# Optimization experiments

Measured on AMD Instinct MI355X. Metric: run time of the kernel, lower is better.

The kernel has to match this reference:

```python
import jax, jax.numpy as jnp
import numpy as np

D_IN = 768
D_OUT = 768
NUM_HEADS = 12
HEAD_DIM = D_OUT // NUM_HEADS


def setup_inputs() -> dict:
    key = jax.random.key(0)
    ks = jax.random.split(key, 6)
    s = 1.0 / np.sqrt(D_IN)
    X = jax.random.normal(ks[0], (4, 2048, D_IN), dtype=jnp.float32)
    Wq = jax.random.uniform(ks[1], (D_IN, D_OUT), jnp.float32, -s, s)
    Wk = jax.random.uniform(ks[2], (D_IN, D_OUT), jnp.float32, -s, s)
    Wv = jax.random.uniform(ks[3], (D_IN, D_OUT), jnp.float32, -s, s)
    Wo = jax.random.uniform(ks[4], (D_OUT, D_OUT), jnp.float32, -s, s)
    bo = jax.random.uniform(ks[5], (D_OUT,), jnp.float32, -s, s)
    return {"X": X, "Wq": Wq, "Wk": Wk, "Wv": Wv, "Wo": Wo, "bo": bo}


def reference(X, Wq, Wk, Wv, Wo, bo):
    b, n, _ = X.shape
    # QKV projections, split heads -> [b, h, n, d]
    def split(t):
        return t.reshape(b, n, NUM_HEADS, HEAD_DIM).transpose(0, 2, 1, 3)
    q = split(X @ Wq)
    k = split(X @ Wk)
    v = split(X @ Wv)
    scores = jnp.einsum('bhqd,bhkd->bhqk', q, k) / np.sqrt(HEAD_DIM).astype(np.float32)
    causal = jnp.triu(jnp.ones((n, n), dtype=bool), k=1)
    scores = jnp.where(causal, -jnp.inf, scores)
    attn = jax.nn.softmax(scores, axis=-1)  # dropout p=0 -> identity
    ctx = jnp.einsum('bhqk,bhkd->bhqd', attn, v)
    ctx = ctx.transpose(0, 2, 1, 3).reshape(b, n, D_OUT)
    return ctx @ Wo + bo
```

## Files before the change

### kernel.cpp

```cpp
#include <hip/hip_runtime.h>
#include <stdint.h>

#define B_  4
#define N_  2048
#define D_  768
#define H_  12
#define HD_ 64
#define M_  (B_*N_)

typedef short bf8 __attribute__((ext_vector_type(8)));
typedef float f32x4 __attribute__((ext_vector_type(4)));

static __device__ __forceinline__ unsigned short f2bf(float f) {
    unsigned u = __float_as_uint(f);
    unsigned r = u + 0x7fffu + ((u >> 16) & 1u);
    return (unsigned short)(r >> 16);
}

static __device__ __forceinline__ unsigned pk2bf(float f0, float f1) {
    return ((__float_as_uint(f1) + 0x8000u) & 0xFFFF0000u) |
           ((__float_as_uint(f0) + 0x8000u) >> 16);
}

#if __has_builtin(__builtin_amdgcn_exp2f)
#define EXP2(x) __builtin_amdgcn_exp2f(x)
#else
#define EXP2(x) exp2f(x)
#endif

#define GLOAD_LDS16(gptr, lptr)                                                   \
    __builtin_amdgcn_global_load_lds(                                             \
        (const __attribute__((address_space(1))) void*)(gptr),                    \
        (__attribute__((address_space(3))) void*)(lptr), 16, 0, 0)

#define QSCALE 0.1803368801111204f

__global__ __launch_bounds__(256) void convert_x(const float* __restrict__ X,
                                                 unsigned short* __restrict__ Xb) {
    const size_t i = ((size_t)blockIdx.x * 256 + threadIdx.x) * 8;
    const float4 a = *(const float4*)(X + i);
    const float4 b = *(const float4*)(X + i + 4);
    ushort4 lo, hi;
    lo.x = f2bf(a.x); lo.y = f2bf(a.y); lo.z = f2bf(a.z); lo.w = f2bf(a.w);
    hi.x = f2bf(b.x); hi.y = f2bf(b.y); hi.z = f2bf(b.z); hi.w = f2bf(b.w);
    *(ushort4*)(Xb + i)     = lo;
    *(ushort4*)(Xb + i + 4) = hi;
}

__global__ __launch_bounds__(256) void transpose_w(
    const float* __restrict__ Wq, const float* __restrict__ Wk,
    const float* __restrict__ Wv, const float* __restrict__ Wo,
    unsigned short* __restrict__ Wqt, unsigned short* __restrict__ Wkt,
    unsigned short* __restrict__ Wvt, unsigned short* __restrict__ Wot)
{
    __shared__ float tile[32][33];
    const int z = blockIdx.z;
    const float* W = (z == 0) ? Wq : (z == 1) ? Wk : (z == 2) ? Wv : Wo;
    unsigned short* Wt = (z == 0) ? Wqt : (z == 1) ? Wkt : (z == 2) ? Wvt : Wot;
    const int k0 = blockIdx.x * 32, n0 = blockIdx.y * 32;
    const int tx = threadIdx.x & 31, ty = threadIdx.x >> 5;
    #pragma unroll
    for (int i = 0; i < 4; ++i)
        tile[ty + 8 * i][tx] = W[(size_t)(k0 + ty + 8 * i) * D_ + n0 + tx];
    __syncthreads();
    #pragma unroll
    for (int i = 0; i < 4; ++i)
        Wt[(size_t)(n0 + ty + 8 * i) * D_ + k0 + tx] = f2bf(tile[tx][ty + 8 * i]);
}

__global__ __launch_bounds__(256) void qkv_mfma(
    const unsigned short* __restrict__ Xb,
    const unsigned short* __restrict__ Wqt, const unsigned short* __restrict__ Wkt,
    const unsigned short* __restrict__ Wvt,
    unsigned short* __restrict__ Qb, unsigned short* __restrict__ Kb,
    unsigned short* __restrict__ Vt)
{
    __shared__ unsigned short As[8192];
    __shared__ unsigned short Bs[8192];

    const int t = threadIdx.x;
    const int wave = t >> 6, lane = t & 63;
    const int col = lane & 15, quad = lane >> 4;
    const int wm = (wave & 1) * 64, wn = (wave >> 1) * 64;

    const int orig = blockIdx.x;
    const int wgid = (orig & 7) * 144 + (orig >> 3);
    const int m0  = (wgid / 18) * 128;
    const int nm  = wgid % 18;
    const int mat = nm / 6;
    const int n0  = (nm % 6) * 128;
    const unsigned short* Wt = (mat == 0) ? Wqt : (mat == 1) ? Wkt : Wvt;
    const bool sw = (mat != 2);

    const unsigned short* Ag = Xb + (size_t)(m0 + (t >> 2)) * D_ + (t & 3) * 8;
    const unsigned short* Bg = Wt + (size_t)(n0 + (t >> 2)) * D_ + (t & 3) * 8;
    unsigned short* AsD = As + t * 8;
    unsigned short* BsD = Bs + t * 8;

    f32x4 acc[4][4] = {};

    for (int k0 = 0; k0 < D_; k0 += 64) {
        __syncthreads();
        GLOAD_LDS16(Ag + k0,                        AsD);
        GLOAD_LDS16(Ag + k0 + 32,                   AsD + 4096);
        GLOAD_LDS16(Ag + (size_t)64 * D_ + k0,      AsD + 2048);
        GLOAD_LDS16(Ag + (size_t)64 * D_ + k0 + 32, AsD + 6144);
        GLOAD_LDS16(Bg + k0,                        BsD);
        GLOAD_LDS16(Bg + k0 + 32,                   BsD + 4096);
        GLOAD_LDS16(Bg + (size_t)64 * D_ + k0,      BsD + 2048);
        GLOAD_LDS16(Bg + (size_t)64 * D_ + k0 + 32, BsD + 6144);
        __syncthreads();

        #pragma unroll
        for (int ks = 0; ks < 2; ++ks) {
            bf8 a[4], b[4];
            #pragma unroll
            for (int i = 0; i < 4; ++i)
                a[i] = *(const bf8*)(As + ks * 4096 + (wm + i * 16 + col) * 32 + quad * 8);
            #pragma unroll
            for (int j = 0; j < 4; ++j)
                b[j] = *(const bf8*)(Bs + ks * 4096 + (wn + j * 16 + col) * 32 + quad * 8);
            if (sw) {
                #pragma unroll
                for (int i = 0; i < 4; ++i)
                    #pragma unroll
                    for (int j = 0; j < 4; ++j)
                        acc[i][j] = __builtin_amdgcn_mfma_f32_16x16x32_bf16(b[j], a[i], acc[i][j], 0, 0, 0);
            } else {
                #pragma unroll
                for (int i = 0; i < 4; ++i)
                    #pragma unroll
                    for (int j = 0; j < 4; ++j)
                        acc[i][j] = __builtin_amdgcn_mfma_f32_16x16x32_bf16(a[i], b[j], acc[i][j], 0, 0, 0);
            }
        }
    }

    if (sw) {
        unsigned short* Out = (mat == 0) ? Qb : Kb;
        const float qsc = (mat == 0) ? QSCALE : 1.0f;
        #pragma unroll
        for (int i = 0; i < 4; ++i) {
            const int token = m0 + wm + i * 16 + col;
            const int bb = token >> 11, nn = token & (N_ - 1);
            #pragma unroll
            for (int j = 0; j < 4; ++j) {
                const int n = n0 + wn + j * 16 + quad * 4;
                const int h = n >> 6, d = n & 63;
                ushort4 pk;
                pk.x = f2bf(acc[i][j][0] * qsc);
                pk.y = f2bf(acc[i][j][1] * qsc);
                pk.z = f2bf(acc[i][j][2] * qsc);
                pk.w = f2bf(acc[i][j][3] * qsc);
                *(ushort4*)(Out + ((size_t)(bb * H_ + h) * N_ + nn) * HD_ + d) = pk;
            }
        }
    } else {
        #pragma unroll
        for (int j = 0; j < 4; ++j) {
            const int n = n0 + wn + j * 16 + col;
            const int h = n >> 6, d = n & 63;
            #pragma unroll
            for (int i = 0; i < 4; ++i) {
                const int mb = m0 + wm + i * 16 + quad * 4;
                const int bb = mb >> 11;
                const int nn = mb & (N_ - 1);
                const int nnp = (nn & ~31) | ((quad >> 1) << 4) | ((quad & 1) << 3) |
                                ((i & 1) << 2);
                ushort4 pk;
                pk.x = f2bf(acc[i][j][0]); pk.y = f2bf(acc[i][j][1]);
                pk.z = f2bf(acc[i][j][2]); pk.w = f2bf(acc[i][j][3]);
                *(ushort4*)(Vt + ((size_t)(bb * H_ + h) * HD_ + d) * N_ + nnp) = pk;
            }
        }
    }
}

#define PS 72

static __device__ __forceinline__ void qk_mfma8(
    const bf8 (&ka)[4][2], bf8 qb0, bf8 qb1, f32x4 (&s)[4])
{
    __builtin_amdgcn_s_setprio(1);
    #pragma unroll
    for (int kc = 0; kc < 4; ++kc) {
        s[kc] = __builtin_amdgcn_mfma_f32_16x16x32_bf16(ka[kc][0], qb0, s[kc], 0, 0, 0);
        s[kc] = __builtin_amdgcn_mfma_f32_16x16x32_bf16(ka[kc][1], qb1, s[kc], 0, 0, 0);
    }
    __builtin_amdgcn_s_setprio(0);
}

static __device__ __forceinline__ void softmax_pack(
    const f32x4 (&s)[4], int k0, int q, bool mask, float& lpart,
    bf8& pb0, bf8& pb1, int quad)
{
    float p[4][4];
    if (mask) {
        #pragma unroll
        for (int kc = 0; kc < 4; ++kc)
            #pragma unroll
            for (int r = 0; r < 4; ++r) {
                const int key = k0 + kc * 16 + quad * 4 + r;
                p[kc][r] = EXP2((key > q) ? -INFINITY : s[kc][r]);
            }
    } else {
        #pragma unroll
        for (int kc = 0; kc < 4; ++kc)
            #pragma unroll
            for (int r = 0; r < 4; ++r) p[kc][r] = EXP2(s[kc][r]);
    }

    #pragma unroll
    for (int kc = 0; kc < 4; ++kc)
        #pragma unroll
        for (int r = 0; r < 4; ++r) lpart += p[kc][r];

    uint4 u0, u1;
    u0.x = pk2bf(p[0][0], p[0][1]); u0.y = pk2bf(p[0][2], p[0][3]);
    u0.z = pk2bf(p[1][0], p[1][1]); u0.w = pk2bf(p[1][2], p[1][3]);
    u1.x = pk2bf(p[2][0], p[2][1]); u1.y = pk2bf(p[2][2], p[2][3]);
    u1.z = pk2bf(p[3][0], p[3][1]); u1.w = pk2bf(p[3][2], p[3][3]);
    pb0 = *(bf8*)&u0;
    pb1 = *(bf8*)&u1;
}

static __device__ __forceinline__ void pv_acc(
    bf8 pb0, bf8 pb1, const bf8 (&va)[4][2], f32x4 (&o)[4])
{
    __builtin_amdgcn_s_setprio(1);
    #pragma unroll
    for (int dc = 0; dc < 4; ++dc) {
        o[dc] = __builtin_amdgcn_mfma_f32_16x16x32_bf16(va[dc][0], pb0, o[dc], 0, 0, 0);
        o[dc] = __builtin_amdgcn_mfma_f32_16x16x32_bf16(va[dc][1], pb1, o[dc], 0, 0, 0);
    }
    __builtin_amdgcn_s_setprio(0);
}

__global__ __launch_bounds__(256, 3) void attn_mfma(
    const unsigned short* __restrict__ Qb,
    const unsigned short* __restrict__ Kb,
    const unsigned short* __restrict__ Vt,
    unsigned short* __restrict__ Ctxb)
{
    __shared__ unsigned short Kl[2][64 * PS];
    __shared__ unsigned short Vl[2][64 * PS];

    const int t = threadIdx.x;
    const int wave = t >> 6;
    const int lane = t & 63;
    const int col  = lane & 15;
    const int quad = lane >> 4;

    const int orig = blockIdx.x;
    const int bid  = (orig & 7) * 96 + (orig >> 3);
    const int bh  = bid >> 4;
    const int x   = bid & 15;
    const int tl  = x, th = 31 - x;
    const int q0L = tl * 64 + wave * 16;
    const int q0H = th * 64 + wave * 16;
    const int qL  = q0L + col;
    const int qH  = q0H + col;

    const unsigned short* Kp = Kb + (size_t)bh * N_ * HD_;
    const unsigned short* Vp = Vt + (size_t)bh * HD_ * N_;
    const unsigned short* QpL = Qb + ((size_t)bh * N_ + q0L) * HD_;
    const unsigned short* QpH = Qb + ((size_t)bh * N_ + q0H) * HD_;

    const bf8 qbL0 = *(const bf8*)(QpL + (size_t)col * HD_ + quad * 8);
    const bf8 qbL1 = *(const bf8*)(QpL + (size_t)col * HD_ + 32 + quad * 8);
    const bf8 qbH0 = *(const bf8*)(QpH + (size_t)col * HD_ + quad * 8);
    const bf8 qbH1 = *(const bf8*)(QpH + (size_t)col * HD_ + 32 + quad * 8);

    f32x4 oL[4] = {}, oH[4] = {};
    float lL = 0.f, lH = 0.f;

    const int srow = t >> 3;
    const int scol = (t & 7) * 8;
    const unsigned short* Kg = Kp + (size_t)srow * HD_ + scol;
    const unsigned short* Vg = Vp + (size_t)srow * N_ + scol;
    const int kO0 = srow * PS + scol;
    const int kO1 = (srow + 32) * PS + scol;

    const int iters = 32 - x;

    uint4 kr0 = *(const uint4*)(Kg);
    uint4 kr1 = *(const uint4*)(Kg + (size_t)32 * HD_);
    uint4 vr0 = *(const uint4*)(Vg);
    uint4 vr1 = *(const uint4*)(Vg + (size_t)32 * N_);
    *(uint4*)(Kl[0] + kO0) = kr0;
    *(uint4*)(Kl[0] + kO1) = kr1;
    *(uint4*)(Vl[0] + kO0) = vr0;
    *(uint4*)(Vl[0] + kO1) = vr1;
    kr0 = *(const uint4*)(Kg + (size_t)64 * HD_);
    kr1 = *(const uint4*)(Kg + (size_t)96 * HD_);
    vr0 = *(const uint4*)(Vg + 64);
    vr1 = *(const uint4*)(Vg + (size_t)32 * N_ + 64);

    for (int kt = 0; kt < iters; ++kt) {
        const int k0 = kt * 64;
        const bool actL = (kt <= tl);
        const unsigned short* Kc = Kl[kt & 1];
        const unsigned short* Vc = Vl[kt & 1];
        unsigned short* Kn = Kl[(kt + 1) & 1];
        unsigned short* Vn = Vl[(kt + 1) & 1];

        __syncthreads();

        if (kt + 1 < iters) {
            *(uint4*)(Kn + kO0) = kr0;
            *(uint4*)(Kn + kO1) = kr1;
            *(uint4*)(Vn + kO0) = vr0;
            *(uint4*)(Vn + kO1) = vr1;
        }
        if (kt + 2 < iters) {
            const size_t k2 = (size_t)(kt + 2) * 64;
            kr0 = *(const uint4*)(Kg + k2 * HD_);
            kr1 = *(const uint4*)(Kg + (k2 + 32) * HD_);
            vr0 = *(const uint4*)(Vg + k2);
            vr1 = *(const uint4*)(Vg + (size_t)32 * N_ + k2);
        }

        bf8 ka[4][2];
        #pragma unroll
        for (int kc = 0; kc < 4; ++kc) {
            ka[kc][0] = *(const bf8*)(Kc + (kc * 16 + col) * PS + quad * 8);
            ka[kc][1] = *(const bf8*)(Kc + (kc * 16 + col) * PS + 32 + quad * 8);
        }

        bf8 va[4][2];
        #pragma unroll
        for (int dc = 0; dc < 4; ++dc) {
            va[dc][0] = *(const bf8*)(Vc + (dc * 16 + col) * PS + quad * 8);
            va[dc][1] = *(const bf8*)(Vc + (dc * 16 + col) * PS + 32 + quad * 8);
        }

        f32x4 sH[4] = {};
        qk_mfma8(ka, qbH0, qbH1, sH);
        f32x4 sL[4] = {};
        if (actL) qk_mfma8(ka, qbL0, qbL1, sL);

        bf8 pbH0, pbH1;
        softmax_pack(sH, k0, qH, kt == th, lH, pbH0, pbH1, quad);
        pv_acc(pbH0, pbH1, va, oH);

        if (actL) {
            bf8 pbL0, pbL1;
            softmax_pack(sL, k0, qL, kt == tl, lL, pbL0, pbL1, quad);
            pv_acc(pbL0, pbL1, va, oL);
        }
    }

    const int b = bh / H_;
    const int h = bh % H_;
    {
        float l = lH;
        l += __shfl_xor(l, 16, 64);
        l += __shfl_xor(l, 32, 64);
        const float inv = 1.0f / l;
        unsigned short* cp = Ctxb + ((size_t)(b * N_ + qH)) * D_ + h * HD_;
        #pragma unroll
        for (int dc = 0; dc < 4; ++dc) {
            uint2 pk;
            pk.x = pk2bf(oH[dc][0] * inv, oH[dc][1] * inv);
            pk.y = pk2bf(oH[dc][2] * inv, oH[dc][3] * inv);
            *(uint2*)(cp + dc * 16 + quad * 4) = pk;
        }
    }
    {
        float l = lL;
        l += __shfl_xor(l, 16, 64);
        l += __shfl_xor(l, 32, 64);
        const float inv = 1.0f / l;
        unsigned short* cp = Ctxb + ((size_t)(b * N_ + qL)) * D_ + h * HD_;
        #pragma unroll
        for (int dc = 0; dc < 4; ++dc) {
            uint2 pk;
            pk.x = pk2bf(oL[dc][0] * inv, oL[dc][1] * inv);
            pk.y = pk2bf(oL[dc][2] * inv, oL[dc][3] * inv);
            *(uint2*)(cp + dc * 16 + quad * 4) = pk;
        }
    }
}

__global__ __launch_bounds__(256) void out_mfma(
    const unsigned short* __restrict__ Ctxb,
    const unsigned short* __restrict__ Wot,
    const float* __restrict__ bo,
    float* __restrict__ Out)
{
    __shared__ unsigned short As[8192];
    __shared__ unsigned short Bs[8192];

    const int t = threadIdx.x;
    const int wave = t >> 6, lane = t & 63;
    const int col = lane & 15, quad = lane >> 4;
    const int wm = (wave & 1) * 64, wn = (wave >> 1) * 64;

    const int orig = blockIdx.x;
    const int wgid = (orig & 7) * 48 + (orig >> 3);
    const int m0 = (wgid / 6) * 128;
    const int n0 = (wgid % 6) * 128;

    const unsigned short* Ag = Ctxb + (size_t)(m0 + (t >> 2)) * D_ + (t & 3) * 8;
    const unsigned short* Bg = Wot + (size_t)(n0 + (t >> 2)) * D_ + (t & 3) * 8;
    unsigned short* AsD = As + t * 8;
    unsigned short* BsD = Bs + t * 8;

    f32x4 acc[4][4] = {};

    for (int k0 = 0; k0 < D_; k0 += 64) {
        __syncthreads();
        GLOAD_LDS16(Ag + k0,                        AsD);
        GLOAD_LDS16(Ag + k0 + 32,                   AsD + 4096);
        GLOAD_LDS16(Ag + (size_t)64 * D_ + k0,      AsD + 2048);
        GLOAD_LDS16(Ag + (size_t)64 * D_ + k0 + 32, AsD + 6144);
        GLOAD_LDS16(Bg + k0,                        BsD);
        GLOAD_LDS16(Bg + k0 + 32,                   BsD + 4096);
        GLOAD_LDS16(Bg + (size_t)64 * D_ + k0,      BsD + 2048);
        GLOAD_LDS16(Bg + (size_t)64 * D_ + k0 + 32, BsD + 6144);
        __syncthreads();

        #pragma unroll
        for (int ks = 0; ks < 2; ++ks) {
            bf8 a[4], b[4];
            #pragma unroll
            for (int i = 0; i < 4; ++i)
                a[i] = *(const bf8*)(As + ks * 4096 + (wm + i * 16 + col) * 32 + quad * 8);
            #pragma unroll
            for (int j = 0; j < 4; ++j)
                b[j] = *(const bf8*)(Bs + ks * 4096 + (wn + j * 16 + col) * 32 + quad * 8);
            #pragma unroll
            for (int i = 0; i < 4; ++i)
                #pragma unroll
                for (int j = 0; j < 4; ++j)
                    acc[i][j] = __builtin_amdgcn_mfma_f32_16x16x32_bf16(b[j], a[i], acc[i][j], 0, 0, 0);
        }
    }

    #pragma unroll
    for (int i = 0; i < 4; ++i) {
        const int m = m0 + wm + i * 16 + col;
        #pragma unroll
        for (int j = 0; j < 4; ++j) {
            const int n = n0 + wn + j * 16 + quad * 4;
            const float4 bias = *(const float4*)(bo + n);
            float4 o;
            o.x = acc[i][j][0] + bias.x;
            o.y = acc[i][j][1] + bias.y;
            o.z = acc[i][j][2] + bias.z;
            o.w = acc[i][j][3] + bias.w;
            *(float4*)(Out + (size_t)m * D_ + n) = o;
        }
    }
}

extern "C" void kernel_launch(void* const* d_in, const int* in_sizes, int n_in,
                              void* d_out, int out_size, void* d_ws, size_t ws_size,
                              hipStream_t stream) {
    const float* X  = (const float*)d_in[0];
    const float* Wq = (const float*)d_in[1];
    const float* Wk = (const float*)d_in[2];
    const float* Wv = (const float*)d_in[3];
    const float* Wo = (const float*)d_in[4];
    const float* bo = (const float*)d_in[5];
    float* out = (float*)d_out;

    const size_t elems = (size_t)M_ * D_;
    const size_t welems = (size_t)D_ * D_;
    unsigned short* Xb  = (unsigned short*)d_ws;
    unsigned short* Wqt = Xb + elems;
    unsigned short* Wkt = Wqt + welems;
    unsigned short* Wvt = Wkt + welems;
    unsigned short* Wot = Wvt + welems;
    unsigned short* Qb  = Wot + welems;
    unsigned short* Kb  = Qb + elems;
    unsigned short* Vt  = Kb + elems;
    unsigned short* Ctxb = Xb;

    convert_x<<<dim3(elems / 2048), 256, 0, stream>>>(X, Xb);
    transpose_w<<<dim3(24, 24, 4), 256, 0, stream>>>(Wq, Wk, Wv, Wo, Wqt, Wkt, Wvt, Wot);

    qkv_mfma<<<dim3(1152), 256, 0, stream>>>(Xb, Wqt, Wkt, Wvt, Qb, Kb, Vt);

    attn_mfma<<<dim3(B_ * H_ * 16), 256, 0, stream>>>(Qb, Kb, Vt, Ctxb);

    out_mfma<<<dim3(384), 256, 0, stream>>>(Ctxb, Wot, bo, out);
}
```

Baseline: 210.1 us.

## Double-buffer LDS tiles in QKV and output projection GEMMs

Both projection GEMM kernels now keep two LDS buffers per operand. The next K-tile is loaded through the direct global-to-LDS path while MFMAs run on the current tile, and there is one barrier per iteration instead of two. The aim is to hide global load latency behind compute. In exchange, LDS use per block doubles to 64KB, which may reduce occupancy. Correctness depends on the explicit waitcnt plus barrier ordering: buffer reuse is only safe because of the trailing barrier.

```diff
diff --git a/kernel.cpp b/kernel.cpp
--- a/kernel.cpp
+++ b/kernel.cpp
@@ -75,8 +75,8 @@
     unsigned short* __restrict__ Qb, unsigned short* __restrict__ Kb,
     unsigned short* __restrict__ Vt)
 {
-    __shared__ unsigned short As[8192];
-    __shared__ unsigned short Bs[8192];
+    __shared__ unsigned short As[2][8192];
+    __shared__ unsigned short Bs[2][8192];
 
     const int t = threadIdx.x;
     const int wave = t >> 6, lane = t & 63;
@@ -94,32 +94,44 @@
 
     const unsigned short* Ag = Xb + (size_t)(m0 + (t >> 2)) * D_ + (t & 3) * 8;
     const unsigned short* Bg = Wt + (size_t)(n0 + (t >> 2)) * D_ + (t & 3) * 8;
-    unsigned short* AsD = As + t * 8;
-    unsigned short* BsD = Bs + t * 8;
+    unsigned short* AsD = &As[0][0] + t * 8;
+    unsigned short* BsD = &Bs[0][0] + t * 8;
+
+#define QKV_STAGE(bsel, kk)                                                        \
+    do {                                                                           \
+        GLOAD_LDS16(Ag + (kk),                        AsD + (bsel) * 8192);        \
+        GLOAD_LDS16(Ag + (kk) + 32,                   AsD + (bsel) * 8192 + 4096); \
+        GLOAD_LDS16(Ag + (size_t)64 * D_ + (kk),      AsD + (bsel) * 8192 + 2048); \
+        GLOAD_LDS16(Ag + (size_t)64 * D_ + (kk) + 32, AsD + (bsel) * 8192 + 6144); \
+        GLOAD_LDS16(Bg + (kk),                        BsD + (bsel) * 8192);        \
+        GLOAD_LDS16(Bg + (kk) + 32,                   BsD + (bsel) * 8192 + 4096); \
+        GLOAD_LDS16(Bg + (size_t)64 * D_ + (kk),      BsD + (bsel) * 8192 + 2048); \
+        GLOAD_LDS16(Bg + (size_t)64 * D_ + (kk) + 32, BsD + (bsel) * 8192 + 6144); \
+    } while (0)
 
     f32x4 acc[4][4] = {};
 
-    for (int k0 = 0; k0 < D_; k0 += 64) {
-        __syncthreads();
-        GLOAD_LDS16(Ag + k0,                        AsD);
-        GLOAD_LDS16(Ag + k0 + 32,                   AsD + 4096);
-        GLOAD_LDS16(Ag + (size_t)64 * D_ + k0,      AsD + 2048);
-        GLOAD_LDS16(Ag + (size_t)64 * D_ + k0 + 32, AsD + 6144);
-        GLOAD_LDS16(Bg + k0,                        BsD);
-        GLOAD_LDS16(Bg + k0 + 32,                   BsD + 4096);
-        GLOAD_LDS16(Bg + (size_t)64 * D_ + k0,      BsD + 2048);
-        GLOAD_LDS16(Bg + (size_t)64 * D_ + k0 + 32, BsD + 6144);
-        __syncthreads();
-
+    QKV_STAGE(0, 0);
+    asm volatile("s_waitcnt vmcnt(0)" ::: "memory");
+    __builtin_amdgcn_s_barrier();
+    __builtin_amdgcn_sched_barrier(0);
+
+    #pragma unroll 2
+    for (int it = 0; it < 12; ++it) {
+        const int cur = it & 1;
+        if (it + 1 < 12) QKV_STAGE(cur ^ 1, (it + 1) * 64);
+
+        const unsigned short* Ab = &As[cur][0];
+        const unsigned short* Bb = &Bs[cur][0];
         #pragma unroll
         for (int ks = 0; ks < 2; ++ks) {
             bf8 a[4], b[4];
             #pragma unroll
             for (int i = 0; i < 4; ++i)
-                a[i] = *(const bf8*)(As + ks * 4096 + (wm + i * 16 + col) * 32 + quad * 8);
+                a[i] = *(const bf8*)(Ab + ks * 4096 + (wm + i * 16 + col) * 32 + quad * 8);
             #pragma unroll
             for (int j = 0; j < 4; ++j)
-                b[j] = *(const bf8*)(Bs + ks * 4096 + (wn + j * 16 + col) * 32 + quad * 8);
+                b[j] = *(const bf8*)(Bb + ks * 4096 + (wn + j * 16 + col) * 32 + quad * 8);
             if (sw) {
                 #pragma unroll
                 for (int i = 0; i < 4; ++i)
@@ -134,7 +146,12 @@
                         acc[i][j] = __builtin_amdgcn_mfma_f32_16x16x32_bf16(a[i], b[j], acc[i][j], 0, 0, 0);
             }
         }
-    }
+
+        asm volatile("s_waitcnt vmcnt(0)" ::: "memory");
+        __builtin_amdgcn_s_barrier();
+        __builtin_amdgcn_sched_barrier(0);
+    }
+#undef QKV_STAGE
 
     if (sw) {
         unsigned short* Out = (mat == 0) ? Qb : Kb;
@@ -388,8 +405,8 @@
     const float* __restrict__ bo,
     float* __restrict__ Out)
 {
-    __shared__ unsigned short As[8192];
-    __shared__ unsigned short Bs[8192];
+    __shared__ unsigned short As[2][8192];
+    __shared__ unsigned short Bs[2][8192];
 
     const int t = threadIdx.x;
     const int wave = t >> 6, lane = t & 63;
@@ -403,39 +420,56 @@
 
     const unsigned short* Ag = Ctxb + (size_t)(m0 + (t >> 2)) * D_ + (t & 3) * 8;
     const unsigned short* Bg = Wot + (size_t)(n0 + (t >> 2)) * D_ + (t & 3) * 8;
-    unsigned short* AsD = As + t * 8;
-    unsigned short* BsD = Bs + t * 8;
+    unsigned short* AsD = &As[0][0] + t * 8;
+    unsigned short* BsD = &Bs[0][0] + t * 8;
+
+#define OUT_STAGE(bsel, kk)                                                        \
+    do {                                                                           \
+        GLOAD_LDS16(Ag + (kk),                        AsD + (bsel) * 8192);        \
+        GLOAD_LDS16(Ag + (kk) + 32,                   AsD + (bsel) * 8192 + 4096); \
+        GLOAD_LDS16(Ag + (size_t)64 * D_ + (kk),      AsD + (bsel) * 8192 + 2048); \
+        GLOAD_LDS16(Ag + (size_t)64 * D_ + (kk) + 32, AsD + (bsel) * 8192 + 6144); \
+        GLOAD_LDS16(Bg + (kk),                        BsD + (bsel) * 8192);        \
+        GLOAD_LDS16(Bg + (kk) + 32,                   BsD + (bsel) * 8192 + 4096); \
+        GLOAD_LDS16(Bg + (size_t)64 * D_ + (kk),      BsD + (bsel) * 8192 + 2048); \
+        GLOAD_LDS16(Bg + (size_t)64 * D_ + (kk) + 32, BsD + (bsel) * 8192 + 6144); \
+    } while (0)
 
     f32x4 acc[4][4] = {};
 
-    for (int k0 = 0; k0 < D_; k0 += 64) {
-        __syncthreads();
-        GLOAD_LDS16(Ag + k0,                        AsD);
-        GLOAD_LDS16(Ag + k0 + 32,                   AsD + 4096);
-        GLOAD_LDS16(Ag + (size_t)64 * D_ + k0,      AsD + 2048);
-        GLOAD_LDS16(Ag + (size_t)64 * D_ + k0 + 32, AsD + 6144);
-        GLOAD_LDS16(Bg + k0,                        BsD);
-        GLOAD_LDS16(Bg + k0 + 32,                   BsD + 4096);
-        GLOAD_LDS16(Bg + (size_t)64 * D_ + k0,      BsD + 2048);
-        GLOAD_LDS16(Bg + (size_t)64 * D_ + k0 + 32, BsD + 6144);
-        __syncthreads();
-
+    OUT_STAGE(0, 0);
+    asm volatile("s_waitcnt vmcnt(0)" ::: "memory");
+    __builtin_amdgcn_s_barrier();
+    __builtin_amdgcn_sched_barrier(0);
+
+    #pragma unroll 2
+    for (int it = 0; it < 12; ++it) {
+        const int cur = it & 1;
+        if (it + 1 < 12) OUT_STAGE(cur ^ 1, (it + 1) * 64);
+
+        const unsigned short* Ab = &As[cur][0];
+        const unsigned short* Bb = &Bs[cur][0];
         #pragma unroll
         for (int ks = 0; ks < 2; ++ks) {
             bf8 a[4], b[4];
             #pragma unroll
             for (int i = 0; i < 4; ++i)
-                a[i] = *(const bf8*)(As + ks * 4096 + (wm + i * 16 + col) * 32 + quad * 8);
+                a[i] = *(const bf8*)(Ab + ks * 4096 + (wm + i * 16 + col) * 32 + quad * 8);
             #pragma unroll
             for (int j = 0; j < 4; ++j)
-                b[j] = *(const bf8*)(Bs + ks * 4096 + (wn + j * 16 + col) * 32 + quad * 8);
+                b[j] = *(const bf8*)(Bb + ks * 4096 + (wn + j * 16 + col) * 32 + quad * 8);
             #pragma unroll
             for (int i = 0; i < 4; ++i)
                 #pragma unroll
                 for (int j = 0; j < 4; ++j)
                     acc[i][j] = __builtin_amdgcn_mfma_f32_16x16x32_bf16(b[j], a[i], acc[i][j], 0, 0, 0);
         }
-    }
+
+        asm volatile("s_waitcnt vmcnt(0)" ::: "memory");
+        __builtin_amdgcn_s_barrier();
+        __builtin_amdgcn_sched_barrier(0);
+    }
+#undef OUT_STAGE
 
     #pragma unroll
     for (int i = 0; i < 4; ++i) {
```

Measured after the change: 203.4 us. 1.03x faster.
